# Performance work log

Measured on AMD Instinct MI355X. Metric: run time of the kernel, lower is better.

## Reference

```python
import jax, jax.numpy as jnp
import numpy as np

EMBED_DIM = 1024
NUM_HEADS = 16
HEAD_DIM = EMBED_DIM // NUM_HEADS


def setup_inputs() -> dict:
    key = jax.random.key(0)
    ks = jax.random.split(key, 9)
    B, T, C = 2, 2048, EMBED_DIM
    s = 1.0 / np.sqrt(C)
    return {
        "x": jax.random.normal(ks[0], (B, T, C), dtype=jnp.float32),
        "Wq": jax.random.normal(ks[1], (C, C), dtype=jnp.float32) * s,
        "bq": jnp.zeros((C,), dtype=jnp.float32),
        "Wk": jax.random.normal(ks[2], (C, C), dtype=jnp.float32) * s,
        "bk": jnp.zeros((C,), dtype=jnp.float32),
        "Wv": jax.random.normal(ks[3], (C, C), dtype=jnp.float32) * s,
        "bv": jnp.zeros((C,), dtype=jnp.float32),
        "Wo": jax.random.normal(ks[4], (C, C), dtype=jnp.float32) * s,
        "bo": jnp.zeros((C,), dtype=jnp.float32),
    }


def reference(x, Wq, bq, Wk, bk, Wv, bv, Wo, bo):
    B, T, C = x.shape
    H, D = NUM_HEADS, HEAD_DIM
    # projections (torch Linear: x @ W.T + b; here W stored as [in,out])
    q = (x @ Wq + bq).reshape(B, T, H, D).transpose(0, 2, 1, 3)  # [B,H,T,D]
    k = (x @ Wk + bk).reshape(B, T, H, D).transpose(0, 2, 1, 3)
    v = (x @ Wv + bv).reshape(B, T, H, D).transpose(0, 2, 1, 3)
    scores = jnp.einsum("bhtd,bhsd->bhts", q, k) / jnp.sqrt(jnp.float32(D))
    causal = jnp.tril(jnp.ones((T, T), dtype=bool))  # keep lower triangle
    scores = jnp.where(causal, scores, -jnp.inf)
    weights = jax.nn.softmax(scores, axis=-1)
    attended = jnp.einsum("bhts,bhsd->bhtd", weights, v)
    attended = attended.transpose(0, 2, 1, 3).reshape(B, T, C)
    return attended @ Wo + bo
```

## Files before the change

kernel.cpp:

```cpp
#include <hip/hip_runtime.h>
#include <math.h>


#define BLOCK 256

typedef __attribute__((ext_vector_type(8))) short bf16x8;
typedef __attribute__((ext_vector_type(4))) float f32x4;
typedef __attribute__((ext_vector_type(16))) float f32x16;

__device__ inline short f2bf(float f) {
  union { float f; unsigned u; } c; c.f = f;
  unsigned u = c.u;
  unsigned r = (u + 0x7fffu + ((u >> 16) & 1u)) >> 16;
  return (short)r;
}

#define GLD_LDS16(g, l)                                            \
  __builtin_amdgcn_global_load_lds(                                \
      (const __attribute__((address_space(1))) unsigned int*)(g),  \
      (__attribute__((address_space(3))) unsigned int*)(l), 16, 0, 0)


__global__ void cvt_all_kernel(const float* __restrict__ x,
                               const float* __restrict__ Wq, const float* __restrict__ Wk,
                               const float* __restrict__ Wv, const float* __restrict__ Wo,
                               short* __restrict__ xb,
                               short* __restrict__ Wtqkv, short* __restrict__ Wto) {
  int z = blockIdx.z;
  if (z >= 4) {
    int blk = blockIdx.x + (blockIdx.y << 5) + ((z - 4) << 10);
    int i = (blk * 256 + threadIdx.x) * 8;
    float4 a = *(const float4*)(x + i);
    float4 b = *(const float4*)(x + i + 4);
    alignas(16) short o[8];
    o[0] = f2bf(a.x); o[1] = f2bf(a.y); o[2] = f2bf(a.z); o[3] = f2bf(a.w);
    o[4] = f2bf(b.x); o[5] = f2bf(b.y); o[6] = f2bf(b.z); o[7] = f2bf(b.w);
    *(int4*)(xb + i) = *(int4*)o;
    return;
  }
  __shared__ float tile[32][33];
  const float* W = (z == 0) ? Wq : (z == 1) ? Wk : (z == 2) ? Wv : Wo;
  short* outp = (z == 3) ? Wto : (Wtqkv + (size_t)z * 1024 * 1024);
  int k0 = blockIdx.x * 32, n0 = blockIdx.y * 32;
  int tr = threadIdx.x >> 5, tc = threadIdx.x & 31;
#pragma unroll
  for (int i = 0; i < 4; i++)
    tile[tr + i * 8][tc] = W[(k0 + tr + i * 8) * 1024 + n0 + tc];
  __syncthreads();
#pragma unroll
  for (int i = 0; i < 4; i++)
    outp[(n0 + tr + i * 8) * 1024 + k0 + tc] = f2bf(tile[tc][tr + i * 8]);
}


__global__ __launch_bounds__(BLOCK) void gemm_qkv_kernel(
    const short* __restrict__ A, const short* __restrict__ Wt,
    const float* __restrict__ bq, const float* __restrict__ bk,
    const float* __restrict__ bv,
    short* __restrict__ Qo, short* __restrict__ Ko, short* __restrict__ Vo) {
  const int Kd = 1024;
  const float QSCL = 0.18033688011f;
  int m0 = blockIdx.x * 128, n0 = blockIdx.y * 128;
  int t = threadIdx.x;
  int lane = t & 63, wv = t >> 6;
  int quad = lane >> 4, lc = lane & 15;
  int wy = wv >> 1, wx = wv & 1;
  __shared__ short As[2][128 * 32];
  __shared__ short Bs[2][128 * 32];
  f32x4 acc[4][4] = {};
  int r0 = t >> 2, c0 = (t & 3) * 8;
  const short* Arow0 = A + (size_t)(m0 + r0) * Kd + c0;
  const short* Arow1 = A + (size_t)(m0 + r0 + 64) * Kd + c0;
  const short* Brow0 = Wt + (size_t)(n0 + r0) * Kd + c0;
  const short* Brow1 = Wt + (size_t)(n0 + r0 + 64) * Kd + c0;
  GLD_LDS16(Arow0, &As[0][8 * t]);
  GLD_LDS16(Arow1, &As[0][8 * t + 2048]);
  GLD_LDS16(Brow0, &Bs[0][8 * t]);
  GLD_LDS16(Brow1, &Bs[0][8 * t + 2048]);
  int cur = 0;
  for (int k0 = 0; k0 < Kd; k0 += 32) {
    __syncthreads();
    if (k0 + 32 < Kd) {
      int nxt = cur ^ 1;
      GLD_LDS16(Arow0 + k0 + 32, &As[nxt][8 * t]);
      GLD_LDS16(Arow1 + k0 + 32, &As[nxt][8 * t + 2048]);
      GLD_LDS16(Brow0 + k0 + 32, &Bs[nxt][8 * t]);
      GLD_LDS16(Brow1 + k0 + 32, &Bs[nxt][8 * t + 2048]);
    }
    bf16x8 af[4], bf[4];
#pragma unroll
    for (int i = 0; i < 4; i++)
      af[i] = *(const bf16x8*)&As[cur][(wy * 64 + i * 16 + lc) * 32 + quad * 8];
#pragma unroll
    for (int i = 0; i < 4; i++)
      bf[i] = *(const bf16x8*)&Bs[cur][(wx * 64 + i * 16 + lc) * 32 + quad * 8];
#pragma unroll
    for (int mi = 0; mi < 4; mi++)
#pragma unroll
      for (int ni = 0; ni < 4; ni++)
        acc[mi][ni] = __builtin_amdgcn_mfma_f32_16x16x32_bf16(af[mi], bf[ni], acc[mi][ni], 0, 0, 0);
    cur ^= 1;
  }
#pragma unroll
  for (int mi = 0; mi < 4; mi++) {
    int row = m0 + wy * 64 + mi * 16 + quad * 4;
#pragma unroll
    for (int ni = 0; ni < 4; ni++) {
      int col = n0 + wx * 64 + ni * 16 + lc;
      int which = col >> 10;
      int hd = col & 1023;
      int h = hd >> 6, d = hd & 63;
      float bb = (which == 0) ? bq[hd] : (which == 1) ? bk[hd] : bv[hd];
      if (which == 2) {
        alignas(8) short pk[4];
#pragma unroll
        for (int r = 0; r < 4; r++) pk[r] = f2bf(acc[mi][ni][r] + bb);
        int b = row >> 11, tt = row & 2047;
        *(int2*)&Vo[((size_t)(b * 16 + h) * 64 + d) * 2048 + tt] = *(const int2*)pk;
      } else {
#pragma unroll
        for (int r = 0; r < 4; r++) {
          int rw = row + r;
          int b = rw >> 11, tt = rw & 2047;
          float val = acc[mi][ni][r] + bb;
          if (which == 0) {
            Qo[((size_t)(b * 16 + h) * 2048 + tt) * 64 + d] = f2bf(val * QSCL);
          } else {
            Ko[((size_t)(b * 16 + h) * 2048 + tt) * 64 + d] = f2bf(val);
          }
        }
      }
    }
  }
}


__global__ __launch_bounds__(BLOCK) void gemm_out_kernel(
    const short* __restrict__ A, const short* __restrict__ Wt,
    const float* __restrict__ bias, float* __restrict__ Out) {
  const int Kd = 1024;
  int m0 = blockIdx.x * 64, n0 = blockIdx.y * 128;
  int t = threadIdx.x;
  int lane = t & 63, wv = t >> 6;
  int quad = lane >> 4, lc = lane & 15;
  int wy = wv >> 1, wx = wv & 1;
  __shared__ short As[2][64 * 32];
  __shared__ short Bs[2][128 * 32];
  int r0 = t >> 2, c0 = (t & 3) * 8;
  f32x4 acc[2][4] = {};
  const short* Arow0 = A + (size_t)(m0 + r0) * Kd + c0;
  const short* Brow0 = Wt + (size_t)(n0 + r0) * Kd + c0;
  const short* Brow1 = Wt + (size_t)(n0 + r0 + 64) * Kd + c0;
  GLD_LDS16(Arow0, &As[0][8 * t]);
  GLD_LDS16(Brow0, &Bs[0][8 * t]);
  GLD_LDS16(Brow1, &Bs[0][8 * t + 2048]);
  int cur = 0;
  for (int k0 = 0; k0 < Kd; k0 += 32) {
    __syncthreads();
    if (k0 + 32 < Kd) {
      int nxt = cur ^ 1;
      GLD_LDS16(Arow0 + k0 + 32, &As[nxt][8 * t]);
      GLD_LDS16(Brow0 + k0 + 32, &Bs[nxt][8 * t]);
      GLD_LDS16(Brow1 + k0 + 32, &Bs[nxt][8 * t + 2048]);
    }
    bf16x8 af[2], bf[4];
#pragma unroll
    for (int i = 0; i < 2; i++)
      af[i] = *(const bf16x8*)&As[cur][(wy * 32 + i * 16 + lc) * 32 + quad * 8];
#pragma unroll
    for (int i = 0; i < 4; i++)
      bf[i] = *(const bf16x8*)&Bs[cur][(wx * 64 + i * 16 + lc) * 32 + quad * 8];
#pragma unroll
    for (int mi = 0; mi < 2; mi++)
#pragma unroll
      for (int ni = 0; ni < 4; ni++)
        acc[mi][ni] = __builtin_amdgcn_mfma_f32_16x16x32_bf16(af[mi], bf[ni], acc[mi][ni], 0, 0, 0);
    cur ^= 1;
  }
#pragma unroll
  for (int mi = 0; mi < 2; mi++) {
    int row = m0 + wy * 32 + mi * 16 + quad * 4;
#pragma unroll
    for (int ni = 0; ni < 4; ni++) {
      int col = n0 + wx * 64 + ni * 16 + lc;
      float bb = bias[col];
#pragma unroll
      for (int r = 0; r < 4; r++)
        Out[(size_t)(row + r) * 1024 + col] = acc[mi][ni][r] + bb;
    }
  }
}


__global__ __launch_bounds__(BLOCK, 2) void attn_kernel(
    const short* __restrict__ Q, const short* __restrict__ K,
    const short* __restrict__ Vt, short* __restrict__ Oa) {
  int p = blockIdx.x;
  int bh = ((p & 7) << 2) | ((p >> 3) & 3);
  int pair = p >> 5;
  int t = threadIdx.x;
  int lane = t & 63, w = t >> 6;
  int qh = w & 1, kh = w >> 1;
  int ln = lane & 31, lh = lane >> 5;
  const short* Qb = Q + (size_t)bh * 2048 * 64;
  const short* Kb = K + (size_t)bh * 2048 * 64;
  const short* Vg = Vt + (size_t)bh * 64 * 2048;
  int b = bh >> 4, h = bh & 15;

  __shared__ short Kt[2][64 * 64];
  __shared__ short Vs[2][64 * 64];
  __shared__ __align__(16) short Ps[4][32 * 72];
  __shared__ float lx[2][64];
  short* Pw = Ps[w];

  int srow = t >> 3;
  int sw = t & 7;
  const float M2 = 14.5f;
  int xk = ln & 7;

  for (int sp = 0; sp < 2; sp++) {
    int s = sp ? (31 - pair) : pair;
    int q0 = s * 64;
    int q0w = q0 + qh * 32;
    int qmaxw = q0w + 31;
    int ntiles = s + 1;

    bf16x8 qf[4];
#pragma unroll
    for (int c = 0; c < 4; c++)
      qf[c] = *(const bf16x8*)&Qb[(size_t)(q0w + ln) * 64 + c * 16 + lh * 8];

    f32x16 O0 = {}, O1 = {};
    float lsum = 0.f;

#pragma unroll
    for (int i = 0; i < 2; i++) {
      int r = i * 32 + srow;
      int cg = sw ^ (r & 7);
      GLD_LDS16(&Kb[(size_t)r * 64 + cg * 8], &Kt[0][i * 2048 + 8 * t]);
      GLD_LDS16(&Vg[(size_t)r * 2048 + cg * 8], &Vs[0][i * 2048 + 8 * t]);
    }
    int cur = 0;
    for (int kt = 0; kt < ntiles; kt++) {
      __syncthreads();
      if (kt + 1 < ntiles) {
        int kb2 = (kt + 1) * 64;
        int nxt = cur ^ 1;
#pragma unroll
        for (int i = 0; i < 2; i++) {
          int r = i * 32 + srow;
          int cg = sw ^ (r & 7);
          GLD_LDS16(&Kb[(size_t)(kb2 + r) * 64 + cg * 8], &Kt[nxt][i * 2048 + 8 * t]);
          GLD_LDS16(&Vg[(size_t)r * 2048 + kb2 + cg * 8], &Vs[nxt][i * 2048 + 8 * t]);
        }
      }
      int grpbase = kt * 64 + kh * 32;
      if (grpbase <= qmaxw) {
        f32x16 S = {};
#pragma unroll
        for (int c = 0; c < 4; c++) {
          int ch = c * 2 + lh;
          bf16x8 kf = *(const bf16x8*)&Kt[cur][(kh * 32 + ln) * 64 + (ch ^ xk) * 8];
          S = __builtin_amdgcn_mfma_f32_32x32x16_bf16(kf, qf[c], S, 0, 0, 0);
        }
        if (kt == ntiles - 1) {
          int qg = q0w + ln;
#pragma unroll
          for (int reg = 0; reg < 16; reg++) {
            int key = grpbase + (reg & 3) + 8 * (reg >> 2) + 4 * lh;
            if (key > qg) S[reg] = -3.0e38f;
          }
        }
#pragma unroll
        for (int g = 0; g < 4; g++) {
          unsigned u[4];
#pragma unroll
          for (int i = 0; i < 4; i++) {
            union { float f; unsigned v; } cc;
            cc.f = __builtin_amdgcn_exp2f(S[g * 4 + i] - M2);
            lsum += cc.f;
            u[i] = cc.v + 0x8000u;
          }
          int2 pk;
          pk.x = (int)__builtin_amdgcn_perm(u[1], u[0], 0x07060302);
          pk.y = (int)__builtin_amdgcn_perm(u[3], u[2], 0x07060302);
          *(int2*)&Pw[ln * 72 + g * 8 + lh * 4] = pk;
        }
#pragma unroll
        for (int c2 = 0; c2 < 2; c2++) {
          bf16x8 pf = *(const bf16x8*)&Pw[ln * 72 + c2 * 16 + lh * 8];
          int ch = kh * 4 + c2 * 2 + lh;
          bf16x8 v0 = *(const bf16x8*)&Vs[cur][ln * 64 + (ch ^ xk) * 8];
          bf16x8 v1 = *(const bf16x8*)&Vs[cur][(32 + ln) * 64 + (ch ^ xk) * 8];
          O0 = __builtin_amdgcn_mfma_f32_32x32x16_bf16(v0, pf, O0, 0, 0, 0);
          O1 = __builtin_amdgcn_mfma_f32_32x32x16_bf16(v1, pf, O1, 0, 0, 0);
        }
      }
      cur ^= 1;
    }

    float* ob = (float*)&Ps[0][0];
    __syncthreads();
    if (kh == 1) {
      float* obw = ob + qh * 2048;
#pragma unroll
      for (int dh = 0; dh < 2; dh++)
#pragma unroll
        for (int reg = 0; reg < 16; reg++)
          obw[((dh * 16 + reg) * 2 + lh) * 32 + ln] = dh ? O1[reg] : O0[reg];
      lx[qh][lane] = lsum;
    }
    __syncthreads();
    if (kh == 0) {
      float* obw = ob + qh * 2048;
#pragma unroll
      for (int reg = 0; reg < 16; reg++) {
        O0[reg] += obw[((0 * 16 + reg) * 2 + lh) * 32 + ln];
        O1[reg] += obw[((1 * 16 + reg) * 2 + lh) * 32 + ln];
      }
      float lt = lsum + lx[qh][lane];
      lt += __shfl_xor(lt, 32, 64);
      float inv = 1.0f / lt;
      size_t rowbase = (size_t)(b * 2048 + q0w + ln) * 1024 + h * 64;
#pragma unroll
      for (int dh = 0; dh < 2; dh++)
#pragma unroll
        for (int g = 0; g < 4; g++) {
          alignas(8) short pk[4];
#pragma unroll
          for (int i = 0; i < 4; i++) {
            float v = dh ? O1[g * 4 + i] : O0[g * 4 + i];
            pk[i] = f2bf(v * inv);
          }
          *(int2*)&Oa[rowbase + dh * 32 + g * 8 + lh * 4] = *(const int2*)pk;
        }
    }
  }
}


extern "C" void kernel_launch(void* const* d_in, const int* in_sizes, int n_in,
                              void* d_out, int out_size, void* d_ws, size_t ws_size,
                              hipStream_t stream) {
  const float* x = (const float*)d_in[0];
  const float* Wq = (const float*)d_in[1];
  const float* bq = (const float*)d_in[2];
  const float* Wk = (const float*)d_in[3];
  const float* bk = (const float*)d_in[4];
  const float* Wv = (const float*)d_in[5];
  const float* bv = (const float*)d_in[6];
  const float* Wo = (const float*)d_in[7];
  const float* bo = (const float*)d_in[8];
  char* ws = (char*)d_ws;
  const size_t MB = 1024 * 1024;
  short* xb = (short*)(ws);
  short* Wtqkv = (short*)(ws + 8 * MB);
  short* Wto = (short*)(ws + 14 * MB);
  short* Qb = (short*)(ws + 17 * MB);
  short* Kb = (short*)(ws + 25 * MB);
  short* Vb = (short*)(ws + 33 * MB);
  short* Att = (short*)(ws + 41 * MB);
  float* out = (float*)d_out;

  cvt_all_kernel<<<dim3(32, 32, 6), BLOCK, 0, stream>>>(x, Wq, Wk, Wv, Wo, xb, Wtqkv, Wto);
  gemm_qkv_kernel<<<dim3(32, 24), BLOCK, 0, stream>>>(xb, Wtqkv, bq, bk, bv, Qb, Kb, Vb);
  attn_kernel<<<512, BLOCK, 0, stream>>>(Qb, Kb, Vb, Att);
  gemm_out_kernel<<<dim3(64, 8), BLOCK, 0, stream>>>(Att, Wto, bo, out);
}
```

Before: 186.5 us.

## Triple-buffer QKV GEMM with XOR-swizzled LDS and XCD-aware tile mapping

The QKV projection GEMM moves from double- to triple-buffered LDS staging, using explicit vmcnt waits so two tiles stay in flight. The global-to-LDS column offsets are XOR-swizzled and the fragment reads use the matching swizzle, to cut LDS bank conflicts. The 2D grid is flattened to 1D and remapped so the blocks on each XCD cover a contiguous region of M and N for L2 reuse. This raises LDS use per block, which may lower occupancy, and the hand-written waitcnt depends on the exact count of outstanding loads.

```diff
diff --git a/kernel.cpp b/kernel.cpp
--- a/kernel.cpp
+++ b/kernel.cpp
@@ -60,47 +60,59 @@
     short* __restrict__ Qo, short* __restrict__ Ko, short* __restrict__ Vo) {
   const int Kd = 1024;
   const float QSCL = 0.18033688011f;
-  int m0 = blockIdx.x * 128, n0 = blockIdx.y * 128;
+  int p = blockIdx.x;
+  int xcd = p & 7, j = p >> 3;
+  int m0 = ((xcd & 3) * 8 + (j & 7)) * 128;
+  int n0 = ((xcd >> 2) * 12 + (j >> 3)) * 128;
   int t = threadIdx.x;
   int lane = t & 63, wv = t >> 6;
   int quad = lane >> 4, lc = lane & 15;
   int wy = wv >> 1, wx = wv & 1;
-  __shared__ short As[2][128 * 32];
-  __shared__ short Bs[2][128 * 32];
+  __shared__ short As[3][128 * 32];
+  __shared__ short Bs[3][128 * 32];
   f32x4 acc[4][4] = {};
-  int r0 = t >> 2, c0 = (t & 3) * 8;
-  const short* Arow0 = A + (size_t)(m0 + r0) * Kd + c0;
-  const short* Arow1 = A + (size_t)(m0 + r0 + 64) * Kd + c0;
-  const short* Brow0 = Wt + (size_t)(n0 + r0) * Kd + c0;
-  const short* Brow1 = Wt + (size_t)(n0 + r0 + 64) * Kd + c0;
-  GLD_LDS16(Arow0, &As[0][8 * t]);
-  GLD_LDS16(Arow1, &As[0][8 * t + 2048]);
-  GLD_LDS16(Brow0, &Bs[0][8 * t]);
-  GLD_LDS16(Brow1, &Bs[0][8 * t + 2048]);
-  int cur = 0;
-  for (int k0 = 0; k0 < Kd; k0 += 32) {
-    __syncthreads();
-    if (k0 + 32 < Kd) {
-      int nxt = cur ^ 1;
-      GLD_LDS16(Arow0 + k0 + 32, &As[nxt][8 * t]);
-      GLD_LDS16(Arow1 + k0 + 32, &As[nxt][8 * t + 2048]);
-      GLD_LDS16(Brow0 + k0 + 32, &Bs[nxt][8 * t]);
-      GLD_LDS16(Brow1 + k0 + 32, &Bs[nxt][8 * t + 2048]);
-    }
+  int r0 = t >> 2;
+  int cs = ((t & 3) ^ ((r0 >> 1) & 3)) * 8;
+  const short* Arow0 = A + (size_t)(m0 + r0) * Kd + cs;
+  const short* Arow1 = A + (size_t)(m0 + r0 + 64) * Kd + cs;
+  const short* Brow0 = Wt + (size_t)(n0 + r0) * Kd + cs;
+  const short* Brow1 = Wt + (size_t)(n0 + r0 + 64) * Kd + cs;
+#define STAGE_QKV(buf, koff)                           \
+  do {                                                 \
+    GLD_LDS16(Arow0 + (koff), &As[buf][8 * t]);        \
+    GLD_LDS16(Arow1 + (koff), &As[buf][8 * t + 2048]); \
+    GLD_LDS16(Brow0 + (koff), &Bs[buf][8 * t]);        \
+    GLD_LDS16(Brow1 + (koff), &Bs[buf][8 * t + 2048]); \
+  } while (0)
+  STAGE_QKV(0, 0);
+  asm volatile("" ::: "memory");
+  STAGE_QKV(1, 32);
+  int xq8 = (quad ^ ((lc >> 1) & 3)) * 8;
+  int cur = 0, wr = 2;
+  for (int step = 0; step < 32; step++) {
+    if (step < 30)
+      asm volatile("s_waitcnt vmcnt(4) lgkmcnt(0)" ::: "memory");
+    else
+      asm volatile("s_waitcnt vmcnt(0) lgkmcnt(0)" ::: "memory");
+    __builtin_amdgcn_s_barrier();
+    asm volatile("" ::: "memory");
+    if (step + 2 < 32) STAGE_QKV(wr, (step + 2) * 32);
     bf16x8 af[4], bf[4];
 #pragma unroll
     for (int i = 0; i < 4; i++)
-      af[i] = *(const bf16x8*)&As[cur][(wy * 64 + i * 16 + lc) * 32 + quad * 8];
+      af[i] = *(const bf16x8*)&As[cur][(wy * 64 + i * 16 + lc) * 32 + xq8];
 #pragma unroll
     for (int i = 0; i < 4; i++)
-      bf[i] = *(const bf16x8*)&Bs[cur][(wx * 64 + i * 16 + lc) * 32 + quad * 8];
+      bf[i] = *(const bf16x8*)&Bs[cur][(wx * 64 + i * 16 + lc) * 32 + xq8];
 #pragma unroll
     for (int mi = 0; mi < 4; mi++)
 #pragma unroll
       for (int ni = 0; ni < 4; ni++)
         acc[mi][ni] = __builtin_amdgcn_mfma_f32_16x16x32_bf16(af[mi], bf[ni], acc[mi][ni], 0, 0, 0);
-    cur ^= 1;
-  }
+    cur = (cur == 2) ? 0 : cur + 1;
+    wr = (wr == 2) ? 0 : wr + 1;
+  }
+#undef STAGE_QKV
 #pragma unroll
   for (int mi = 0; mi < 4; mi++) {
     int row = m0 + wy * 64 + mi * 16 + quad * 4;
@@ -363,7 +375,7 @@
   float* out = (float*)d_out;
 
   cvt_all_kernel<<<dim3(32, 32, 6), BLOCK, 0, stream>>>(x, Wq, Wk, Wv, Wo, xb, Wtqkv, Wto);
-  gemm_qkv_kernel<<<dim3(32, 24), BLOCK, 0, stream>>>(xb, Wtqkv, bq, bk, bv, Qb, Kb, Vb);
+  gemm_qkv_kernel<<<dim3(768), BLOCK, 0, stream>>>(xb, Wtqkv, bq, bk, bv, Qb, Kb, Vb);
   attn_kernel<<<512, BLOCK, 0, stream>>>(Qb, Kb, Vb, Att);
   gemm_out_kernel<<<dim3(64, 8), BLOCK, 0, stream>>>(Att, Wto, bo, out);
 }
```

Result: slower. 196.3 us (+5.2%).
